# Kernel optimization log

Measured on AMD Instinct MI355X. Metric: run time of the kernel, lower is better.

The kernel has to match this reference:

```python
import jax, jax.numpy as jnp
import numpy as np

LATENT = 512
CIN = 512
COUT = 512
K = 3
B, H, W = 16, 64, 64

# equalized-lr multipliers (use_wscale=True, lrmul=1, gain=1)
W_MUL_CONV = (CIN * K * K) ** (-0.5)
W_MUL_DENSE = LATENT ** (-0.5)


def setup_inputs() -> dict:
    key = jax.random.key(0)
    k1, k2, k3, k4 = jax.random.split(key, 4)
    x = jax.random.normal(k1, (B, CIN, H, W), dtype=jnp.float32)
    y = jax.random.normal(k2, (B, LATENT), dtype=jnp.float32)
    dense_w = jax.random.normal(k3, (CIN, LATENT), dtype=jnp.float32)
    dense_b = jnp.ones((CIN,), dtype=jnp.float32)  # style bias, init 1 (StyleGAN2)
    weight = jax.random.normal(k4, (COUT, CIN, K, K), dtype=jnp.float32)
    return {"x": x, "y": y, "dense_w": dense_w, "dense_b": dense_b, "weight": weight}


def reference(x, y, dense_w, dense_b, weight):
    # style: s[b, cin] = (y @ dense_w.T) * w_mul + bias (linear bias_act)
    s = jnp.einsum('bl,cl->bc', y, dense_w) * W_MUL_DENSE + dense_b  # [B, Cin]

    # modulate: per-sample weights ww[b,o,i,kh,kw]
    w = weight * W_MUL_CONV
    ww = w[None] * s[:, None, :, None, None]  # [B, Cout, Cin, K, K]

    # demodulate
    d = jax.lax.rsqrt(jnp.sum(ww * ww, axis=(2, 3, 4)) + 1e-8)  # [B, Cout]
    ww = ww * d[:, :, None, None, None]

    # fused grouped conv: groups = B, VALID padding (F.conv2d default)
    b = x.shape[0]
    x_g = x.reshape(1, b * CIN, H, W)
    w_g = ww.reshape(b * COUT, CIN, K, K)
    out = jax.lax.conv_general_dilated(
        x_g, w_g,
        window_strides=(1, 1), padding='VALID',
        dimension_numbers=('NCHW', 'OIHW', 'NCHW'),
        feature_group_count=b)
    return out.reshape(b, COUT, H - K + 1, W - K + 1)
```

## Files before the change

kernel.cpp:

```cpp
#include <hip/hip_runtime.h>
#include <hip/hip_bf16.h>

#define CIN 512
#define COUT 512
#define BATCH 16
#define NP 3844
#define OW 62

#define W_MUL_DENSE 0.044194173824159216f
#define W_MUL_CONV  0.014731391274719736f

using short8  = __attribute__((ext_vector_type(8))) short;
using floatx4 = __attribute__((ext_vector_type(4))) float;
using uintx4  = __attribute__((ext_vector_type(4))) unsigned int;

__device__ __forceinline__ unsigned short f2bfu(float f) {
    unsigned u = __builtin_bit_cast(unsigned, f);
    u += 0x7FFFu + ((u >> 16) & 1u);
    return (unsigned short)(u >> 16);
}

__device__ __forceinline__ void gload_lds16(const void* g, void* l) {
    __builtin_amdgcn_global_load_lds(
        (const __attribute__((address_space(1))) void*)g,
        (__attribute__((address_space(3))) void*)l, 16, 0, 0);
}


__global__ void emc_style_kernel(const float* __restrict__ y, const float* __restrict__ dw,
                                 const float* __restrict__ db, float* __restrict__ s) {
    int idx = blockIdx.x * 256 + threadIdx.x;
    int b = idx >> 9, c = idx & 511;
    const float4* yb = (const float4*)(y + b * 512);
    const float4* wc = (const float4*)(dw + c * 512);
    float acc = 0.f;
#pragma unroll 4
    for (int l = 0; l < 128; ++l) {
        float4 a = yb[l], w4 = wc[l];
        acc += a.x * w4.x + a.y * w4.y + a.z * w4.z + a.w * w4.w;
    }
    s[idx] = acc * W_MUL_DENSE + db[c];
}

__global__ void emc_wsq_kernel(const float* __restrict__ w, float* __restrict__ wsq) {
    int idx = blockIdx.x * 256 + threadIdx.x;
    const float* p = w + (size_t)idx * 9;
    float a = 0.f;
#pragma unroll
    for (int j = 0; j < 9; ++j) a += p[j] * p[j];
    wsq[idx] = a;
}

__global__ void emc_demod_kernel(const float* __restrict__ s, const float* __restrict__ wsq,
                                 float* __restrict__ d) {
    int idx = blockIdx.x * 256 + threadIdx.x;
    int b = idx >> 9, o = idx & 511;
    const float4* sb = (const float4*)(s + b * 512);
    const float4* wo = (const float4*)(wsq + o * 512);
    float acc = 0.f;
#pragma unroll 4
    for (int l = 0; l < 128; ++l) {
        float4 a = sb[l], c = wo[l];
        acc += a.x * a.x * c.x + a.y * a.y * c.y + a.z * a.z * c.z + a.w * a.w * c.w;
    }
    d[idx] = rsqrtf(W_MUL_CONV * W_MUL_CONV * acc + 1e-8f);
}

__global__ void emc_wrepack_kernel(const float* __restrict__ w, unsigned short* __restrict__ wb) {
    int idx = blockIdx.x * 256 + threadIdx.x;
    int i = idx & 511;
    int r = idx >> 9;
    int kpos = r % 9;
    int o = r / 9;
    wb[idx] = f2bfu(w[(size_t)(o * 512 + i) * 9 + kpos]);
}


__global__ __launch_bounds__(256, 3) void emc_conv_kernel(
    const float* __restrict__ x, const unsigned short* __restrict__ wb,
    const float* __restrict__ sv, const float* __restrict__ dv,
    float* __restrict__ out) {

    __shared__ __align__(16) unsigned short smA[2][128 * 32];
    __shared__ __align__(16) unsigned short smB[260 * 40];
    __shared__ float s_s[512];
    __shared__ float s_d[128];

    int orig = blockIdx.x;
    int cpx = gridDim.x >> 3;
    int bid = (orig & 7) * cpx + (orig >> 3);

    int b = bid / 124;
    int t = bid - b * 124;
    int ot = t & 3;
    int strip = t >> 2;
    int oB = ot * 128;
    int r0 = strip * 2;

    int tid = threadIdx.x;
    int lane = tid & 63;
    int wid = tid >> 6;

    s_s[tid]       = sv[b * 512 + tid];
    s_s[tid + 256] = sv[b * 512 + 256 + tid];
    if (tid < 128) s_d[tid] = dv[b * 512 + oB + tid];

    int sc = tid & 63;
    int sr = tid >> 6;
    const float* xrow = x + (size_t)b * (512 * 4096) + (r0 + sr) * 64 + sc;
    unsigned short* bg = smB + (sr * 64 + sc) * 40;

    const unsigned short* asrc[2];
#pragma unroll
    for (int j = 0; j < 2; ++j)
        asrc[j] = wb + (size_t)(oB + (wid * 2 + j) * 16 + (lane >> 2)) * 4608 + (lane & 3) * 8;

    int frc = lane & 15, q = lane >> 4;
    int wr = wid >> 1, wc = wid & 1;
    int aidx[4], bidx[4];
#pragma unroll
    for (int m = 0; m < 4; ++m) aidx[m] = (wr * 64 + m * 16 + frc) * 32 + q * 8;
#pragma unroll
    for (int n = 0; n < 4; ++n) bidx[n] = (wc * 64 + n * 16 + frc) * 40 + q * 8;

    floatx4 acc[4][4];
#pragma unroll
    for (int m = 0; m < 4; ++m)
#pragma unroll
        for (int n = 0; n < 4; ++n) acc[m][n] = floatx4{0.f, 0.f, 0.f, 0.f};

    unsigned held[16];

    __syncthreads();

#pragma unroll
    for (int j = 0; j < 2; ++j)
        gload_lds16(asrc[j], &smA[0][(wid * 2 + j) * 512]);

#pragma unroll
    for (int sl = 0; sl < 8; ++sl) {
        const float* xp = xrow + (size_t)(sl * 4) * 4096;
        int i0 = sl * 4;
        float v0 = xp[0]         * s_s[i0];
        float v1 = xp[4096]      * s_s[i0 + 1];
        float v2 = xp[2 * 4096]  * s_s[i0 + 2];
        float v3 = xp[3 * 4096]  * s_s[i0 + 3];
        held[2 * sl]     = (unsigned)f2bfu(v0) | ((unsigned)f2bfu(v1) << 16);
        held[2 * sl + 1] = (unsigned)f2bfu(v2) | ((unsigned)f2bfu(v3) << 16);
    }
    *(uintx4*)(bg)      = uintx4{held[0],  held[1],  held[2],  held[3]};
    *(uintx4*)(bg + 8)  = uintx4{held[4],  held[5],  held[6],  held[7]};
    *(uintx4*)(bg + 16) = uintx4{held[8],  held[9],  held[10], held[11]};
    *(uintx4*)(bg + 24) = uintx4{held[12], held[13], held[14], held[15]};

    __syncthreads();

    for (int itile = 0; itile < 16; ++itile) {
        const float* xit = xrow + (size_t)(itile + 1) * 32 * 4096;
        int sbase = (itile + 1) * 32;
        int cur = itile & 1;
#pragma unroll
        for (int kpos = 0; kpos < 9; ++kpos) {
            int abuf = (cur + kpos) & 1;
            if (!(itile == 15 && kpos == 8)) {
                int kN = (kpos == 8) ? 0 : kpos + 1;
                int iN = (kpos == 8) ? itile + 1 : itile;
                int off = kN * 512 + iN * 32;
#pragma unroll
                for (int j = 0; j < 2; ++j)
                    gload_lds16(asrc[j] + off, &smA[abuf ^ 1][(wid * 2 + j) * 512]);
            }
            if (kpos < 8 && itile < 15) {
                const float* xp = xit + (size_t)(kpos * 4) * 4096;
                int i0 = sbase + kpos * 4;
                float v0 = xp[0]        * s_s[i0];
                float v1 = xp[4096]     * s_s[i0 + 1];
                float v2 = xp[2 * 4096] * s_s[i0 + 2];
                float v3 = xp[3 * 4096] * s_s[i0 + 3];
                held[2 * kpos]     = (unsigned)f2bfu(v0) | ((unsigned)f2bfu(v1) << 16);
                held[2 * kpos + 1] = (unsigned)f2bfu(v2) | ((unsigned)f2bfu(v3) << 16);
            }
            {
                int kh = kpos / 3, kw = kpos - kh * 3;
                int bo = (kh * 64 + kw) * 40;
                const unsigned short* A = smA[abuf];
                short8 af[4], bfr[4];
#pragma unroll
                for (int m = 0; m < 4; ++m) af[m] = *(const short8*)(A + aidx[m]);
#pragma unroll
                for (int n = 0; n < 4; ++n) bfr[n] = *(const short8*)(smB + bidx[n] + bo);
#pragma unroll
                for (int m = 0; m < 4; ++m)
#pragma unroll
                    for (int n = 0; n < 4; ++n)
                        acc[m][n] = __builtin_amdgcn_mfma_f32_16x16x32_bf16(af[m], bfr[n], acc[m][n], 0, 0, 0);
            }
            if (kpos == 8) {
                __syncthreads();
                if (itile < 15) {
                    *(uintx4*)(bg)      = uintx4{held[0],  held[1],  held[2],  held[3]};
                    *(uintx4*)(bg + 8)  = uintx4{held[4],  held[5],  held[6],  held[7]};
                    *(uintx4*)(bg + 16) = uintx4{held[8],  held[9],  held[10], held[11]};
                    *(uintx4*)(bg + 24) = uintx4{held[12], held[13], held[14], held[15]};
                }
                __syncthreads();
            } else {
                __syncthreads();
            }
        }
    }

    size_t outb = (size_t)b * 512 * NP;
#pragma unroll
    for (int m = 0; m < 4; ++m) {
#pragma unroll
        for (int r = 0; r < 4; ++r) {
            int o_l = wr * 64 + m * 16 + q * 4 + r;
            float scale = W_MUL_CONV * s_d[o_l];
            size_t rb = outb + (size_t)(oB + o_l) * NP + strip * 124 + wc * OW;
#pragma unroll
            for (int n = 0; n < 4; ++n) {
                int col = n * 16 + frc;
                if (col < OW) out[rb + col] = acc[m][n][r] * scale;
            }
        }
    }
}

extern "C" void kernel_launch(void* const* d_in, const int* in_sizes, int n_in,
                              void* d_out, int out_size, void* d_ws, size_t ws_size,
                              hipStream_t stream) {
    const float* x  = (const float*)d_in[0];
    const float* y  = (const float*)d_in[1];
    const float* dw = (const float*)d_in[2];
    const float* db = (const float*)d_in[3];
    const float* w  = (const float*)d_in[4];
    float* out = (float*)d_out;

    char* ws = (char*)d_ws;
    float* s_  = (float*)ws;
    float* d_  = (float*)(ws + 32768);
    float* wsq = (float*)(ws + 65536);
    unsigned short* wb = (unsigned short*)(ws + 65536 + 1048576);

    emc_style_kernel<<<32, 256, 0, stream>>>(y, dw, db, s_);
    emc_wsq_kernel<<<1024, 256, 0, stream>>>(w, wsq);
    emc_demod_kernel<<<32, 256, 0, stream>>>(s_, wsq, d_);
    emc_wrepack_kernel<<<9216, 256, 0, stream>>>(w, wb);
    emc_conv_kernel<<<16 * 124, 256, 0, stream>>>(x, wb, s_, d_, out);
}
```

Measured before the change: 401.3 us.

## Double output-channel tile to 256 and XOR-swizzle weight LDS layout

Each conv block now covers 256 output channels instead of 128, so every wave holds an 8x4 MFMA accumulator grid. This halves the grid and halves how often the modulated input tile is built per output channel, reusing each B fragment across twice as many MFMAs. The weight tile in LDS gets an XOR swizzle on the 16-byte chunk index to cut bank conflicts on fragment reads. In exchange, register pressure roughly doubles for accumulators (launch bounds drop to 2 blocks/SM) and the grid shrinks to 992 blocks, which lowers occupancy and latency hiding.

```diff
diff --git a/kernel.cpp b/kernel.cpp
--- a/kernel.cpp
+++ b/kernel.cpp
@@ -76,25 +76,25 @@
 }
 
 
-__global__ __launch_bounds__(256, 3) void emc_conv_kernel(
+__global__ __launch_bounds__(256, 2) void emc_conv_kernel(
     const float* __restrict__ x, const unsigned short* __restrict__ wb,
     const float* __restrict__ sv, const float* __restrict__ dv,
     float* __restrict__ out) {
 
-    __shared__ __align__(16) unsigned short smA[2][128 * 32];
+    __shared__ __align__(16) unsigned short smA[2][256 * 32];
     __shared__ __align__(16) unsigned short smB[260 * 40];
     __shared__ float s_s[512];
-    __shared__ float s_d[128];
+    __shared__ float s_d[256];
 
     int orig = blockIdx.x;
     int cpx = gridDim.x >> 3;
     int bid = (orig & 7) * cpx + (orig >> 3);
 
-    int b = bid / 124;
-    int t = bid - b * 124;
-    int ot = t & 3;
-    int strip = t >> 2;
-    int oB = ot * 128;
+    int b = bid / 62;
+    int t = bid - b * 62;
+    int ot = t & 1;
+    int strip = t >> 1;
+    int oB = ot * 256;
     int r0 = strip * 2;
 
     int tid = threadIdx.x;
@@ -103,29 +103,36 @@
 
     s_s[tid]       = sv[b * 512 + tid];
     s_s[tid + 256] = sv[b * 512 + 256 + tid];
-    if (tid < 128) s_d[tid] = dv[b * 512 + oB + tid];
+    s_d[tid]       = dv[b * 512 + oB + tid];
 
     int sc = tid & 63;
     int sr = tid >> 6;
     const float* xrow = x + (size_t)b * (512 * 4096) + (r0 + sr) * 64 + sc;
     unsigned short* bg = smB + (sr * 64 + sc) * 40;
 
-    const unsigned short* asrc[2];
-#pragma unroll
-    for (int j = 0; j < 2; ++j)
-        asrc[j] = wb + (size_t)(oB + (wid * 2 + j) * 16 + (lane >> 2)) * 4608 + (lane & 3) * 8;
+    const unsigned short* asrc[4];
+    int adst[4];
+#pragma unroll
+    for (int j = 0; j < 4; ++j) {
+        int row = wid * 64 + j * 16 + (lane >> 2);
+        asrc[j] = wb + (size_t)(oB + row) * 4608 + (((lane & 3) ^ ((row >> 1) & 3)) << 3);
+        adst[j] = (wid * 64 + j * 16) * 32;
+    }
 
     int frc = lane & 15, q = lane >> 4;
     int wr = wid >> 1, wc = wid & 1;
-    int aidx[4], bidx[4];
-#pragma unroll
-    for (int m = 0; m < 4; ++m) aidx[m] = (wr * 64 + m * 16 + frc) * 32 + q * 8;
+    int aidx[8], bidx[4];
+#pragma unroll
+    for (int m = 0; m < 8; ++m) {
+        int row = wr * 128 + m * 16 + frc;
+        aidx[m] = row * 32 + ((q ^ ((row >> 1) & 3)) << 3);
+    }
 #pragma unroll
     for (int n = 0; n < 4; ++n) bidx[n] = (wc * 64 + n * 16 + frc) * 40 + q * 8;
 
-    floatx4 acc[4][4];
-#pragma unroll
-    for (int m = 0; m < 4; ++m)
+    floatx4 acc[8][4];
+#pragma unroll
+    for (int m = 0; m < 8; ++m)
 #pragma unroll
         for (int n = 0; n < 4; ++n) acc[m][n] = floatx4{0.f, 0.f, 0.f, 0.f};
 
@@ -134,8 +141,8 @@
     __syncthreads();
 
 #pragma unroll
-    for (int j = 0; j < 2; ++j)
-        gload_lds16(asrc[j], &smA[0][(wid * 2 + j) * 512]);
+    for (int j = 0; j < 4; ++j)
+        gload_lds16(asrc[j], &smA[0][adst[j]]);
 
 #pragma unroll
     for (int sl = 0; sl < 8; ++sl) {
@@ -167,8 +174,8 @@
                 int iN = (kpos == 8) ? itile + 1 : itile;
                 int off = kN * 512 + iN * 32;
 #pragma unroll
-                for (int j = 0; j < 2; ++j)
-                    gload_lds16(asrc[j] + off, &smA[abuf ^ 1][(wid * 2 + j) * 512]);
+                for (int j = 0; j < 4; ++j)
+                    gload_lds16(asrc[j] + off, &smA[abuf ^ 1][adst[j]]);
             }
             if (kpos < 8 && itile < 15) {
                 const float* xp = xit + (size_t)(kpos * 4) * 4096;
@@ -184,16 +191,21 @@
                 int kh = kpos / 3, kw = kpos - kh * 3;
                 int bo = (kh * 64 + kw) * 40;
                 const unsigned short* A = smA[abuf];
-                short8 af[4], bfr[4];
-#pragma unroll
-                for (int m = 0; m < 4; ++m) af[m] = *(const short8*)(A + aidx[m]);
+                short8 bfr[4];
 #pragma unroll
                 for (int n = 0; n < 4; ++n) bfr[n] = *(const short8*)(smB + bidx[n] + bo);
 #pragma unroll
-                for (int m = 0; m < 4; ++m)
-#pragma unroll
-                    for (int n = 0; n < 4; ++n)
-                        acc[m][n] = __builtin_amdgcn_mfma_f32_16x16x32_bf16(af[m], bfr[n], acc[m][n], 0, 0, 0);
+                for (int mh = 0; mh < 2; ++mh) {
+                    short8 af[4];
+#pragma unroll
+                    for (int mm = 0; mm < 4; ++mm) af[mm] = *(const short8*)(A + aidx[mh * 4 + mm]);
+#pragma unroll
+                    for (int mm = 0; mm < 4; ++mm)
+#pragma unroll
+                        for (int n = 0; n < 4; ++n)
+                            acc[mh * 4 + mm][n] = __builtin_amdgcn_mfma_f32_16x16x32_bf16(
+                                af[mm], bfr[n], acc[mh * 4 + mm][n], 0, 0, 0);
+                }
             }
             if (kpos == 8) {
                 __syncthreads();
@@ -212,10 +224,10 @@
 
     size_t outb = (size_t)b * 512 * NP;
 #pragma unroll
-    for (int m = 0; m < 4; ++m) {
+    for (int m = 0; m < 8; ++m) {
 #pragma unroll
         for (int r = 0; r < 4; ++r) {
-            int o_l = wr * 64 + m * 16 + q * 4 + r;
+            int o_l = wr * 128 + m * 16 + q * 4 + r;
             float scale = W_MUL_CONV * s_d[o_l];
             size_t rb = outb + (size_t)(oB + o_l) * NP + strip * 124 + wc * OW;
 #pragma unroll
@@ -247,5 +259,5 @@
     emc_wsq_kernel<<<1024, 256, 0, stream>>>(w, wsq);
     emc_demod_kernel<<<32, 256, 0, stream>>>(s_, wsq, d_);
     emc_wrepack_kernel<<<9216, 256, 0, stream>>>(w, wb);
-    emc_conv_kernel<<<16 * 124, 256, 0, stream>>>(x, wb, s_, d_, out);
-}
+    emc_conv_kernel<<<16 * 62, 256, 0, stream>>>(x, wb, s_, d_, out);
+}
```

Result: faster. 349.1 us (-13.0%).
